# Kernel optimization log

Hardware: AMD Instinct MI355X
Metric: run time of the kernel (lower is better)

## Reference

```python
import jax, jax.numpy as jnp
import numpy as np

ORDER = 8
POOL = 8
N_SIDE = 1 << ORDER          # 256
N_PIX = N_SIDE * N_SIDE      # 65536
PSQ = POOL * POOL            # 64
CHANNEL = 2 * PSQ            # 128
PATH_NUM = N_PIX // PSQ      # 1024


def hilbert_indices(order):
    """hil[d] = row-major pixel index of the d-th point on the Hilbert curve;
    rehil = inverse permutation (rehil[hil[d]] = d)."""
    n = 1 << order
    d = np.arange(n * n, dtype=np.int64)
    x = np.zeros_like(d)
    y = np.zeros_like(d)
    t = d.copy()
    s = 1
    while s < n:
        rx = 1 & (t // 2)
        ry = 1 & (t ^ rx)
        swap = ry == 0
        flip = swap & (rx == 1)
        x = np.where(flip, s - 1 - x, x)
        y = np.where(flip, s - 1 - y, y)
        x, y = np.where(swap, y, x), np.where(swap, x, y)
        x = x + s * rx
        y = y + s * ry
        t = t // 4
        s *= 2
    hil = (y * n + x).astype(np.int32)
    rehil = np.argsort(hil).astype(np.int32)
    return hil, rehil


def setup_inputs() -> dict:
    key = jax.random.key(0)
    ks = jax.random.split(key, 10)
    b, c = 8, 128
    scale = 1.0 / np.sqrt(CHANNEL)
    hil, rehil = hilbert_indices(ORDER)
    return {
        "x": jax.random.normal(ks[0], (b, c, N_SIDE, N_SIDE), jnp.float32),
        "Wq": jax.random.normal(ks[1], (CHANNEL, CHANNEL), jnp.float32) * scale,
        "bq": jax.random.normal(ks[2], (CHANNEL,), jnp.float32) * 0.01,
        "Wk": jax.random.normal(ks[3], (CHANNEL, CHANNEL), jnp.float32) * scale,
        "bk": jax.random.normal(ks[4], (CHANNEL,), jnp.float32) * 0.01,
        "Wv": jax.random.normal(ks[5], (CHANNEL, CHANNEL), jnp.float32) * scale,
        "bv": jax.random.normal(ks[6], (CHANNEL,), jnp.float32) * 0.01,
        "Wpre": jax.random.normal(ks[7], (1, 2), jnp.float32) * 0.5,
        "bpre": jax.random.normal(ks[8], (1,), jnp.float32) * 0.01,
        "hil": jnp.asarray(hil),
        "rehil": jnp.asarray(rehil),
    }


def reference(x, Wq, bq, Wk, bk, Wv, bv, Wpre, bpre, hil, rehil):
    b, c, h, w = x.shape
    n_pix = h * w
    psq = Wq.shape[0] // 2
    path_num = n_pix // psq

    # channel-pooled descriptor: (b, 2, h*w)
    mean = jnp.mean(x, axis=1)
    mx = jnp.max(x, axis=1)
    x1 = jnp.stack([mean, mx], axis=1).reshape(b, 2, n_pix)

    # Hilbert-curve gather reorder of pixels
    xh = x1[:, :, hil]                                            # (b, 2, n_pix)

    # group psq consecutive curve points into one token of dim 2*psq
    feat = xh.reshape(b, 2, path_num, psq)
    feat = feat.transpose(0, 1, 3, 2).reshape(b, 2 * psq, path_num)  # (b, C, P)

    # 1x1-conv QKV projections
    Q = jnp.einsum('oc,bcp->bop', Wq, feat) + bq[None, :, None]
    K = jnp.einsum('oc,bcp->bop', Wk, feat) + bk[None, :, None]
    V = jnp.einsum('oc,bcp->bop', Wv, feat) + bv[None, :, None]

    # scores[b,p,q] = sum_c Q[b,c,p] * K[b,c,q]; softmax over dim 1 (as nn.Softmax(1))
    scores = jnp.einsum('bcp,bcq->bpq', Q, K)
    a = jax.nn.softmax(scores, axis=1)

    # x3c[b,c,p] = sum_q a[b,p,q] * V[b,c,q]
    x3c = jnp.einsum('bpq,bcq->bcp', a, V)                        # (b, C, P)

    # ungroup tokens back to curve order, then inverse-Hilbert scatter
    back = x3c.reshape(b, 2, psq, path_num).transpose(0, 1, 3, 2).reshape(b, 2, n_pix)
    restored = back[:, :, rehil].reshape(b, 2, h, w)

    # 1x1 conv 2 -> 1, sigmoid gate
    att = jnp.einsum('oc,bchw->bohw', Wpre, restored) + bpre[None, :, None, None]
    return jax.nn.sigmoid(att) * x
```

## Files before the change

### kernel.cpp

```cpp
#include <hip/hip_runtime.h>

#define BATCH 8
#define CH 128
#define NPIX 65536
#define PN 1024

__global__ __launch_bounds__(256) void k0_precompute(
    const float* __restrict__ Wq, const float* __restrict__ bq,
    const float* __restrict__ Wk, const float* __restrict__ bk,
    float* __restrict__ M, float* __restrict__ wqbk,
    float* __restrict__ wkbq, float* __restrict__ c0) {
  int t = blockIdx.x * 256 + threadIdx.x;
  if (t < 16384) {
    int c = t >> 7, c2 = t & 127;
    float s = 0.f;
    for (int o = 0; o < 128; ++o) s += Wq[o * 128 + c] * Wk[o * 128 + c2];
    M[t] = s;
  } else if (t < 16512) {
    int c = t - 16384;
    float s = 0.f;
    for (int o = 0; o < 128; ++o) s += Wq[o * 128 + c] * bk[o];
    wqbk[c] = s;
  } else if (t < 16640) {
    int c = t - 16512;
    float s = 0.f;
    for (int o = 0; o < 128; ++o) s += bq[o] * Wk[o * 128 + c];
    wkbq[c] = s;
  } else if (t == 16640) {
    float s = 0.f;
    for (int o = 0; o < 128; ++o) s += bq[o] * bk[o];
    c0[0] = s;
  }
}

__global__ __launch_bounds__(256) void k1_reduce_permute(
    const float* __restrict__ x, const int* __restrict__ rehil,
    float* __restrict__ F) {
  const int b = blockIdx.y;
  const int t = blockIdx.x * 256 + threadIdx.x;
  const int i0 = t * 4;
  const float* xb = x + (size_t)b * CH * NPIX + i0;
  float4 s = make_float4(0.f, 0.f, 0.f, 0.f);
  float4 m = make_float4(-1e30f, -1e30f, -1e30f, -1e30f);
  for (int c = 0; c < CH; ++c) {
    const float4 v = *(const float4*)(xb + (size_t)c * NPIX);
    s.x += v.x; s.y += v.y; s.z += v.z; s.w += v.w;
    m.x = fmaxf(m.x, v.x); m.y = fmaxf(m.y, v.y);
    m.z = fmaxf(m.z, v.z); m.w = fmaxf(m.w, v.w);
  }
  const float inv = 1.f / (float)CH;
  float mean[4] = {s.x * inv, s.y * inv, s.z * inv, s.w * inv};
  float mx[4] = {m.x, m.y, m.z, m.w};
  const int4 d4 = *(const int4*)(rehil + i0);
  int ds[4] = {d4.x, d4.y, d4.z, d4.w};
  float* Fb = F + (size_t)b * CH * PN;
#pragma unroll
  for (int e = 0; e < 4; ++e) {
    int d = ds[e];
    int p = d >> 6, j = d & 63;
    Fb[j * PN + p] = mean[e];
    Fb[(64 + j) * PN + p] = mx[e];
  }
}

__global__ __launch_bounds__(256) void ku_uv(
    const float* __restrict__ F, const float* __restrict__ wqbk,
    const float* __restrict__ wkbq, float* __restrict__ u, float* __restrict__ v) {
  const int b = blockIdx.y;
  const int p = blockIdx.x * 256 + threadIdx.x;
  const float* Fb = F + (size_t)b * CH * PN;
  float su = 0.f, sv = 0.f;
  for (int c = 0; c < CH; ++c) {
    float f = Fb[c * PN + p];
    su = fmaf(f, wqbk[c], su);
    sv = fmaf(f, wkbq[c], sv);
  }
  u[b * PN + p] = su;
  v[b * PN + p] = sv;
}

__global__ __launch_bounds__(256) void k2_gv(
    const float* __restrict__ M, const float* __restrict__ Wv,
    const float* __restrict__ bv, const float* __restrict__ F,
    float* __restrict__ G, float* __restrict__ Vt) {
  __shared__ float As[16][64];
  __shared__ float Bs[16][64];
  const int b = blockIdx.z;
  const int r0 = blockIdx.y * 64;
  const int q0 = blockIdx.x * 64;
  const float* Fb = F + (size_t)b * CH * PN;
  const int t = threadIdx.x;
  const int tx = t & 15, ty = t >> 4;
  const int arow = t & 63, ak4 = (t >> 6) * 4;
  float acc[4][4] = {};
  for (int k0 = 0; k0 < 128; k0 += 16) {
    const int r = r0 + arow;
    const float* Arow = (r < 128) ? (M + r * 128) : (Wv + (r - 128) * 128);
    float4 a = *(const float4*)(Arow + k0 + ak4);
    As[ak4 + 0][arow] = a.x;
    As[ak4 + 1][arow] = a.y;
    As[ak4 + 2][arow] = a.z;
    As[ak4 + 3][arow] = a.w;
    *(float4*)&Bs[ty][tx * 4] =
        *(const float4*)(Fb + (size_t)(k0 + ty) * PN + q0 + tx * 4);
    __syncthreads();
#pragma unroll
    for (int kk = 0; kk < 16; ++kk) {
      float4 a4 = *(const float4*)&As[kk][ty * 4];
      float4 b4 = *(const float4*)&Bs[kk][tx * 4];
      float av[4] = {a4.x, a4.y, a4.z, a4.w};
      float bw[4] = {b4.x, b4.y, b4.z, b4.w};
#pragma unroll
      for (int i = 0; i < 4; ++i)
#pragma unroll
        for (int j = 0; j < 4; ++j) acc[i][j] = fmaf(av[i], bw[j], acc[i][j]);
    }
    __syncthreads();
  }
  float* Gb = G + (size_t)b * CH * PN;
  float* Vtb = Vt + (size_t)b * PN * CH;
#pragma unroll
  for (int i = 0; i < 4; ++i) {
    const int r = r0 + ty * 4 + i;
#pragma unroll
    for (int j = 0; j < 4; ++j) {
      const int q = q0 + tx * 4 + j;
      if (r < 128) Gb[r * PN + q] = acc[i][j];
      else Vtb[(size_t)q * CH + (r - 128)] = acc[i][j] + bv[r - 128];
    }
  }
}

__global__ __launch_bounds__(256) void k3_scores(
    const float* __restrict__ G, const float* __restrict__ F,
    const float* __restrict__ u, const float* __restrict__ v,
    const float* __restrict__ c0, float* __restrict__ St) {
  __shared__ float As[16][64];
  __shared__ float Bs[16][64];
  const int b = blockIdx.z;
  const int q0 = blockIdx.y * 64;
  const int p0 = blockIdx.x * 64;
  const float* Gb = G + (size_t)b * CH * PN;
  const float* Fb = F + (size_t)b * CH * PN;
  const int t = threadIdx.x;
  const int tx = t & 15, ty = t >> 4;
  float acc[4][4] = {};
  for (int k0 = 0; k0 < 128; k0 += 16) {
    *(float4*)&As[ty][tx * 4] =
        *(const float4*)(Gb + (size_t)(k0 + ty) * PN + q0 + tx * 4);
    *(float4*)&Bs[ty][tx * 4] =
        *(const float4*)(Fb + (size_t)(k0 + ty) * PN + p0 + tx * 4);
    __syncthreads();
#pragma unroll
    for (int kk = 0; kk < 16; ++kk) {
      float4 a4 = *(const float4*)&As[kk][ty * 4];
      float4 b4 = *(const float4*)&Bs[kk][tx * 4];
      float av[4] = {a4.x, a4.y, a4.z, a4.w};
      float bw[4] = {b4.x, b4.y, b4.z, b4.w};
#pragma unroll
      for (int i = 0; i < 4; ++i)
#pragma unroll
        for (int j = 0; j < 4; ++j) acc[i][j] = fmaf(av[i], bw[j], acc[i][j]);
    }
    __syncthreads();
  }
  const float cc = c0[0];
  float* Sb = St + (size_t)b * PN * PN;
#pragma unroll
  for (int i = 0; i < 4; ++i) {
    const int q = q0 + ty * 4 + i;
    const float vq = v[b * PN + q] + cc;
#pragma unroll
    for (int j = 0; j < 4; ++j) {
      const int p = p0 + tx * 4 + j;
      Sb[(size_t)q * PN + p] = acc[i][j] + u[b * PN + p] + vq;
    }
  }
}

__global__ __launch_bounds__(256) void k4_softmax_stats(
    const float* __restrict__ St, float* __restrict__ mOut,
    float* __restrict__ izOut) {
  const int wid = threadIdx.x >> 6;
  const int lane = threadIdx.x & 63;
  const int row = blockIdx.x * 4 + wid;
  const float* Sr = St + (size_t)row * PN;
  float4 r[4];
  float m = -1e30f;
#pragma unroll
  for (int ch = 0; ch < 4; ++ch) {
    r[ch] = *(const float4*)(Sr + ch * 256 + lane * 4);
    m = fmaxf(m, fmaxf(fmaxf(r[ch].x, r[ch].y), fmaxf(r[ch].z, r[ch].w)));
  }
#pragma unroll
  for (int off = 32; off >= 1; off >>= 1) m = fmaxf(m, __shfl_xor(m, off));
  float z = 0.f;
#pragma unroll
  for (int ch = 0; ch < 4; ++ch) {
    z += __expf(r[ch].x - m) + __expf(r[ch].y - m) +
         __expf(r[ch].z - m) + __expf(r[ch].w - m);
  }
#pragma unroll
  for (int off = 32; off >= 1; off >>= 1) z += __shfl_xor(z, off);
  if (lane == 0) {
    mOut[row] = m;
    izOut[row] = 1.f / z;
  }
}

__global__ __launch_bounds__(256) void k5_av(
    const float* __restrict__ Vt, const float* __restrict__ St,
    const float* __restrict__ mIn, const float* __restrict__ izIn,
    float* __restrict__ X3) {
  __shared__ float As[16][64];
  __shared__ float Bs[16][64];
  const int b = blockIdx.z;
  const int c0 = blockIdx.y * 64;
  const int p0 = blockIdx.x * 64;
  const float* Vtb = Vt + (size_t)b * PN * CH;
  const float* Sb = St + (size_t)b * PN * PN;
  const int t = threadIdx.x;
  const int tx = t & 15, ty = t >> 4;
  float acc[4][4] = {};
  for (int k0 = 0; k0 < PN; k0 += 16) {
    const int q = k0 + ty;
    *(float4*)&As[ty][tx * 4] =
        *(const float4*)(Vtb + (size_t)q * CH + c0 + tx * 4);
    const float mq = mIn[b * PN + q];
    const float iz = izIn[b * PN + q];
    const float4 sv = *(const float4*)(Sb + (size_t)q * PN + p0 + tx * 4);
    float4 ev;
    ev.x = __expf(sv.x - mq) * iz;
    ev.y = __expf(sv.y - mq) * iz;
    ev.z = __expf(sv.z - mq) * iz;
    ev.w = __expf(sv.w - mq) * iz;
    *(float4*)&Bs[ty][tx * 4] = ev;
    __syncthreads();
#pragma unroll
    for (int kk = 0; kk < 16; ++kk) {
      float4 a4 = *(const float4*)&As[kk][ty * 4];
      float4 b4 = *(const float4*)&Bs[kk][tx * 4];
      float av[4] = {a4.x, a4.y, a4.z, a4.w};
      float bw[4] = {b4.x, b4.y, b4.z, b4.w};
#pragma unroll
      for (int i = 0; i < 4; ++i)
#pragma unroll
        for (int j = 0; j < 4; ++j) acc[i][j] = fmaf(av[i], bw[j], acc[i][j]);
    }
    __syncthreads();
  }
  float* X3b = X3 + (size_t)b * CH * PN;
#pragma unroll
  for (int i = 0; i < 4; ++i)
#pragma unroll
    for (int j = 0; j < 4; ++j)
      X3b[(size_t)(c0 + ty * 4 + i) * PN + p0 + tx * 4 + j] = acc[i][j];
}

__global__ __launch_bounds__(256) void k7_out(
    const float* __restrict__ x, const int* __restrict__ rehil,
    const float* __restrict__ X3, const float* __restrict__ Wpre,
    const float* __restrict__ bpre, float* __restrict__ out) {
  const int b = blockIdx.y;
  const int t = blockIdx.x * 256 + threadIdx.x;
  const int i0 = t * 4;
  const float w0 = Wpre[0], w1 = Wpre[1], b0 = bpre[0];
  const int4 d4 = *(const int4*)(rehil + i0);
  const float* X3b = X3 + (size_t)b * CH * PN;
  int ds[4] = {d4.x, d4.y, d4.z, d4.w};
  float g[4];
#pragma unroll
  for (int e = 0; e < 4; ++e) {
    const int d = ds[e];
    const int p = d >> 6, j = d & 63;
    const float r0v = X3b[j * PN + p];
    const float r1v = X3b[(64 + j) * PN + p];
    const float logit = fmaf(w0, r0v, fmaf(w1, r1v, b0));
    g[e] = 1.f / (1.f + __expf(-logit));
  }
  const size_t base = (size_t)b * CH * NPIX + i0;
#pragma unroll 4
  for (int c = 0; c < CH; ++c) {
    const float4 v = *(const float4*)(x + base + (size_t)c * NPIX);
    float4 o;
    o.x = v.x * g[0];
    o.y = v.y * g[1];
    o.z = v.z * g[2];
    o.w = v.w * g[3];
    *(float4*)(out + base + (size_t)c * NPIX) = o;
  }
}

extern "C" void kernel_launch(void* const* d_in, const int* in_sizes, int n_in,
                              void* d_out, int out_size, void* d_ws,
                              size_t ws_size, hipStream_t stream) {
  const float* x = (const float*)d_in[0];
  const float* Wq = (const float*)d_in[1];
  const float* bq = (const float*)d_in[2];
  const float* Wk = (const float*)d_in[3];
  const float* bk = (const float*)d_in[4];
  const float* Wv = (const float*)d_in[5];
  const float* bv = (const float*)d_in[6];
  const float* Wpre = (const float*)d_in[7];
  const float* bpre = (const float*)d_in[8];
  const int* rehil = (const int*)d_in[10];
  float* out = (float*)d_out;
  float* ws = (float*)d_ws;

  const size_t SZ_FEAT = (size_t)BATCH * CH * PN;
  float* F = ws;
  float* G = F + SZ_FEAT;
  float* Vt = G + SZ_FEAT;
  float* X3 = Vt + SZ_FEAT;
  float* Mw = X3 + SZ_FEAT;
  float* wqbk = Mw + 16384;
  float* wkbq = wqbk + 128;
  float* c0w = wkbq + 128;
  float* uw = c0w + 64;
  float* vw = uw + 8192;
  float* mw = vw + 8192;
  float* izw = mw + 8192;
  float* Stw = izw + 8192;
  const size_t need = (size_t)(Stw - ws) + (size_t)BATCH * PN * PN;
  float* St = Stw;
  if (ws_size < need * sizeof(float)) {
    St = out;
  }

  k0_precompute<<<66, 256, 0, stream>>>(Wq, bq, Wk, bk, Mw, wqbk, wkbq, c0w);
  k1_reduce_permute<<<dim3(64, BATCH), 256, 0, stream>>>(x, rehil, F);
  ku_uv<<<dim3(4, BATCH), 256, 0, stream>>>(F, wqbk, wkbq, uw, vw);
  k2_gv<<<dim3(16, 4, BATCH), 256, 0, stream>>>(Mw, Wv, bv, F, G, Vt);
  k3_scores<<<dim3(16, 16, BATCH), 256, 0, stream>>>(G, F, uw, vw, c0w, St);
  k4_softmax_stats<<<2048, 256, 0, stream>>>(St, mw, izw);
  k5_av<<<dim3(16, 2, BATCH), 256, 0, stream>>>(Vt, St, mw, izw, X3);
  k7_out<<<dim3(64, BATCH), 256, 0, stream>>>(x, rehil, X3, Wpre, bpre, out);
}
```

Measured before the change: 685.9 us.

## Use 128x128 register tiles and split-K attention-value matmul with separate reduction

```diff
diff --git a/kernel.cpp b/kernel.cpp
--- a/kernel.cpp
+++ b/kernel.cpp
@@ -131,49 +131,64 @@
   }
 }
 
-__global__ __launch_bounds__(256) void k3_scores(
+__global__ __launch_bounds__(256) void k3_scores128(
     const float* __restrict__ G, const float* __restrict__ F,
     const float* __restrict__ u, const float* __restrict__ v,
     const float* __restrict__ c0, float* __restrict__ St) {
-  __shared__ float As[16][64];
-  __shared__ float Bs[16][64];
+  __shared__ float As[16][128];
+  __shared__ float Bs[16][128];
   const int b = blockIdx.z;
-  const int q0 = blockIdx.y * 64;
-  const int p0 = blockIdx.x * 64;
+  const int q0 = blockIdx.y * 128;
+  const int p0 = blockIdx.x * 128;
   const float* Gb = G + (size_t)b * CH * PN;
   const float* Fb = F + (size_t)b * CH * PN;
   const int t = threadIdx.x;
   const int tx = t & 15, ty = t >> 4;
-  float acc[4][4] = {};
+  const int sr = t >> 4;
+  const int sc = (t & 15) * 8;
+  float acc[8][8] = {};
   for (int k0 = 0; k0 < 128; k0 += 16) {
-    *(float4*)&As[ty][tx * 4] =
-        *(const float4*)(Gb + (size_t)(k0 + ty) * PN + q0 + tx * 4);
-    *(float4*)&Bs[ty][tx * 4] =
-        *(const float4*)(Fb + (size_t)(k0 + ty) * PN + p0 + tx * 4);
+    const float* gsrc = Gb + (size_t)(k0 + sr) * PN + q0 + sc;
+    const float* fsrc = Fb + (size_t)(k0 + sr) * PN + p0 + sc;
+    *(float4*)&As[sr][sc] = *(const float4*)gsrc;
+    *(float4*)&As[sr][sc + 4] = *(const float4*)(gsrc + 4);
+    *(float4*)&Bs[sr][sc] = *(const float4*)fsrc;
+    *(float4*)&Bs[sr][sc + 4] = *(const float4*)(fsrc + 4);
     __syncthreads();
 #pragma unroll
     for (int kk = 0; kk < 16; ++kk) {
-      float4 a4 = *(const float4*)&As[kk][ty * 4];
-      float4 b4 = *(const float4*)&Bs[kk][tx * 4];
-      float av[4] = {a4.x, a4.y, a4.z, a4.w};
-      float bw[4] = {b4.x, b4.y, b4.z, b4.w};
-#pragma unroll
-      for (int i = 0; i < 4; ++i)
-#pragma unroll
-        for (int j = 0; j < 4; ++j) acc[i][j] = fmaf(av[i], bw[j], acc[i][j]);
+      float a0[8], b0[8];
+      *(float4*)&a0[0] = *(const float4*)&As[kk][ty * 4];
+      *(float4*)&a0[4] = *(const float4*)&As[kk][64 + ty * 4];
+      *(float4*)&b0[0] = *(const float4*)&Bs[kk][tx * 4];
+      *(float4*)&b0[4] = *(const float4*)&Bs[kk][64 + tx * 4];
+#pragma unroll
+      for (int i = 0; i < 8; ++i)
+#pragma unroll
+        for (int j = 0; j < 8; ++j) acc[i][j] = fmaf(a0[i], b0[j], acc[i][j]);
     }
     __syncthreads();
   }
   const float cc = c0[0];
   float* Sb = St + (size_t)b * PN * PN;
-#pragma unroll
-  for (int i = 0; i < 4; ++i) {
-    const int q = q0 + ty * 4 + i;
-    const float vq = v[b * PN + q] + cc;
-#pragma unroll
-    for (int j = 0; j < 4; ++j) {
-      const int p = p0 + tx * 4 + j;
-      Sb[(size_t)q * PN + p] = acc[i][j] + u[b * PN + p] + vq;
+  const float* ub = u + b * PN;
+  const float* vb = v + b * PN;
+  float4 u0 = *(const float4*)(ub + p0 + tx * 4);
+  float4 u1 = *(const float4*)(ub + p0 + 64 + tx * 4);
+  float ua[8] = {u0.x, u0.y, u0.z, u0.w, u1.x, u1.y, u1.z, u1.w};
+#pragma unroll
+  for (int i = 0; i < 8; ++i) {
+    const int q = q0 + ((i < 4) ? (ty * 4 + i) : (64 + ty * 4 + i - 4));
+    const float vq = vb[q] + cc;
+    float* row = Sb + (size_t)q * PN;
+#pragma unroll
+    for (int jh = 0; jh < 2; ++jh) {
+      float4 o;
+      o.x = acc[i][jh * 4 + 0] + ua[jh * 4 + 0] + vq;
+      o.y = acc[i][jh * 4 + 1] + ua[jh * 4 + 1] + vq;
+      o.z = acc[i][jh * 4 + 2] + ua[jh * 4 + 2] + vq;
+      o.w = acc[i][jh * 4 + 3] + ua[jh * 4 + 3] + vq;
+      *(float4*)(row + p0 + jh * 64 + tx * 4) = o;
     }
   }
 }
@@ -208,59 +223,92 @@
   }
 }
 
-__global__ __launch_bounds__(256) void k5_av(
+__global__ __launch_bounds__(256) void k5_av128(
     const float* __restrict__ Vt, const float* __restrict__ St,
     const float* __restrict__ mIn, const float* __restrict__ izIn,
-    float* __restrict__ X3) {
-  __shared__ float As[16][64];
-  __shared__ float Bs[16][64];
+    float* __restrict__ P) {
+  __shared__ float As[16][128];
+  __shared__ float Bs[16][128];
   const int b = blockIdx.z;
-  const int c0 = blockIdx.y * 64;
-  const int p0 = blockIdx.x * 64;
+  const int part = blockIdx.y;
+  const int p0 = blockIdx.x * 128;
   const float* Vtb = Vt + (size_t)b * PN * CH;
   const float* Sb = St + (size_t)b * PN * PN;
+  const float* mb = mIn + b * PN;
+  const float* izb = izIn + b * PN;
   const int t = threadIdx.x;
   const int tx = t & 15, ty = t >> 4;
-  float acc[4][4] = {};
-  for (int k0 = 0; k0 < PN; k0 += 16) {
-    const int q = k0 + ty;
-    *(float4*)&As[ty][tx * 4] =
-        *(const float4*)(Vtb + (size_t)q * CH + c0 + tx * 4);
-    const float mq = mIn[b * PN + q];
-    const float iz = izIn[b * PN + q];
-    const float4 sv = *(const float4*)(Sb + (size_t)q * PN + p0 + tx * 4);
-    float4 ev;
-    ev.x = __expf(sv.x - mq) * iz;
-    ev.y = __expf(sv.y - mq) * iz;
-    ev.z = __expf(sv.z - mq) * iz;
-    ev.w = __expf(sv.w - mq) * iz;
-    *(float4*)&Bs[ty][tx * 4] = ev;
+  const int sr = t >> 4;
+  const int sc = (t & 15) * 8;
+  float acc[8][8] = {};
+  const int qbase = part * 128;
+  for (int k0 = 0; k0 < 128; k0 += 16) {
+    const int q = qbase + k0 + sr;
+    const float* asrc = Vtb + (size_t)q * CH + sc;
+    *(float4*)&As[sr][sc] = *(const float4*)asrc;
+    *(float4*)&As[sr][sc + 4] = *(const float4*)(asrc + 4);
+    const float mq = mb[q];
+    const float iz = izb[q];
+    const float* ssrc = Sb + (size_t)q * PN + p0 + sc;
+    float4 s0 = *(const float4*)ssrc;
+    float4 s1 = *(const float4*)(ssrc + 4);
+    float4 e0, e1;
+    e0.x = __expf(s0.x - mq) * iz; e0.y = __expf(s0.y - mq) * iz;
+    e0.z = __expf(s0.z - mq) * iz; e0.w = __expf(s0.w - mq) * iz;
+    e1.x = __expf(s1.x - mq) * iz; e1.y = __expf(s1.y - mq) * iz;
+    e1.z = __expf(s1.z - mq) * iz; e1.w = __expf(s1.w - mq) * iz;
+    *(float4*)&Bs[sr][sc] = e0;
+    *(float4*)&Bs[sr][sc + 4] = e1;
     __syncthreads();
 #pragma unroll
     for (int kk = 0; kk < 16; ++kk) {
-      float4 a4 = *(const float4*)&As[kk][ty * 4];
-      float4 b4 = *(const float4*)&Bs[kk][tx * 4];
-      float av[4] = {a4.x, a4.y, a4.z, a4.w};
-      float bw[4] = {b4.x, b4.y, b4.z, b4.w};
-#pragma unroll
-      for (int i = 0; i < 4; ++i)
-#pragma unroll
-        for (int j = 0; j < 4; ++j) acc[i][j] = fmaf(av[i], bw[j], acc[i][j]);
-    }
-    __syncthreads();
-  }
-  float* X3b = X3 + (size_t)b * CH * PN;
-#pragma unroll
-  for (int i = 0; i < 4; ++i)
-#pragma unroll
-    for (int j = 0; j < 4; ++j)
-      X3b[(size_t)(c0 + ty * 4 + i) * PN + p0 + tx * 4 + j] = acc[i][j];
-}
-
-__global__ __launch_bounds__(256) void k7_out(
-    const float* __restrict__ x, const int* __restrict__ rehil,
-    const float* __restrict__ X3, const float* __restrict__ Wpre,
-    const float* __restrict__ bpre, float* __restrict__ out) {
+      float a0[8], b0[8];
+      *(float4*)&a0[0] = *(const float4*)&As[kk][ty * 4];
+      *(float4*)&a0[4] = *(const float4*)&As[kk][64 + ty * 4];
+      *(float4*)&b0[0] = *(const float4*)&Bs[kk][tx * 4];
+      *(float4*)&b0[4] = *(const float4*)&Bs[kk][64 + tx * 4];
+#pragma unroll
+      for (int i = 0; i < 8; ++i)
+#pragma unroll
+        for (int j = 0; j < 8; ++j) acc[i][j] = fmaf(a0[i], b0[j], acc[i][j]);
+    }
+    __syncthreads();
+  }
+  float* Pb = P + ((size_t)(part * BATCH + b) * CH) * PN;
+#pragma unroll
+  for (int i = 0; i < 8; ++i) {
+    const int c = (i < 4) ? (ty * 4 + i) : (64 + ty * 4 + i - 4);
+    float* row = Pb + (size_t)c * PN;
+#pragma unroll
+    for (int jh = 0; jh < 2; ++jh) {
+      float4 o;
+      o.x = acc[i][jh * 4 + 0];
+      o.y = acc[i][jh * 4 + 1];
+      o.z = acc[i][jh * 4 + 2];
+      o.w = acc[i][jh * 4 + 3];
+      *(float4*)(row + p0 + jh * 64 + tx * 4) = o;
+    }
+  }
+}
+
+__global__ __launch_bounds__(256) void k6_reduce(
+    const float* __restrict__ P, float* __restrict__ X3) {
+  const size_t t = (size_t)blockIdx.x * 256 + threadIdx.x;
+  const size_t idx = t * 4;
+  const size_t stride = (size_t)BATCH * CH * PN;
+  float4 s = *(const float4*)(P + idx);
+#pragma unroll
+  for (int part = 1; part < 8; ++part) {
+    const float4 v = *(const float4*)(P + part * stride + idx);
+    s.x += v.x; s.y += v.y; s.z += v.z; s.w += v.w;
+  }
+  *(float4*)(X3 + idx) = s;
+}
+
+__global__ __launch_bounds__(256) void k6g_gate(
+    const float* __restrict__ X3, const int* __restrict__ rehil,
+    const float* __restrict__ Wpre, const float* __restrict__ bpre,
+    float* __restrict__ gate) {
   const int b = blockIdx.y;
   const int t = blockIdx.x * 256 + threadIdx.x;
   const int i0 = t * 4;
@@ -268,7 +316,8 @@
   const int4 d4 = *(const int4*)(rehil + i0);
   const float* X3b = X3 + (size_t)b * CH * PN;
   int ds[4] = {d4.x, d4.y, d4.z, d4.w};
-  float g[4];
+  float4 g;
+  float* gp = &g.x;
 #pragma unroll
   for (int e = 0; e < 4; ++e) {
     const int d = ds[e];
@@ -276,17 +325,27 @@
     const float r0v = X3b[j * PN + p];
     const float r1v = X3b[(64 + j) * PN + p];
     const float logit = fmaf(w0, r0v, fmaf(w1, r1v, b0));
-    g[e] = 1.f / (1.f + __expf(-logit));
-  }
+    gp[e] = 1.f / (1.f + __expf(-logit));
+  }
+  *(float4*)(gate + (size_t)b * NPIX + i0) = g;
+}
+
+__global__ __launch_bounds__(256) void k7_out(
+    const float* __restrict__ x, const float* __restrict__ gate,
+    float* __restrict__ out) {
+  const int b = blockIdx.y;
+  const int t = blockIdx.x * 256 + threadIdx.x;
+  const int i0 = t * 4;
+  const float4 g = *(const float4*)(gate + (size_t)b * NPIX + i0);
   const size_t base = (size_t)b * CH * NPIX + i0;
 #pragma unroll 4
   for (int c = 0; c < CH; ++c) {
     const float4 v = *(const float4*)(x + base + (size_t)c * NPIX);
     float4 o;
-    o.x = v.x * g[0];
-    o.y = v.y * g[1];
-    o.z = v.z * g[2];
-    o.w = v.w * g[3];
+    o.x = v.x * g.x;
+    o.y = v.y * g.y;
+    o.z = v.z * g.z;
+    o.w = v.w * g.w;
     *(float4*)(out + base + (size_t)c * NPIX) = o;
   }
 }
@@ -320,7 +379,9 @@
   float* vw = uw + 8192;
   float* mw = vw + 8192;
   float* izw = mw + 8192;
-  float* Stw = izw + 8192;
+  float* gatew = izw + 8192;
+  float* Pw = gatew + 524288;
+  float* Stw = Pw + 8 * SZ_FEAT;
   const size_t need = (size_t)(Stw - ws) + (size_t)BATCH * PN * PN;
   float* St = Stw;
   if (ws_size < need * sizeof(float)) {
@@ -331,8 +392,10 @@
   k1_reduce_permute<<<dim3(64, BATCH), 256, 0, stream>>>(x, rehil, F);
   ku_uv<<<dim3(4, BATCH), 256, 0, stream>>>(F, wqbk, wkbq, uw, vw);
   k2_gv<<<dim3(16, 4, BATCH), 256, 0, stream>>>(Mw, Wv, bv, F, G, Vt);
-  k3_scores<<<dim3(16, 16, BATCH), 256, 0, stream>>>(G, F, uw, vw, c0w, St);
+  k3_scores128<<<dim3(8, 8, BATCH), 256, 0, stream>>>(G, F, uw, vw, c0w, St);
   k4_softmax_stats<<<2048, 256, 0, stream>>>(St, mw, izw);
-  k5_av<<<dim3(16, 2, BATCH), 256, 0, stream>>>(Vt, St, mw, izw, X3);
-  k7_out<<<dim3(64, BATCH), 256, 0, stream>>>(x, rehil, X3, Wpre, bpre, out);
-}
+  k5_av128<<<dim3(8, 8, BATCH), 256, 0, stream>>>(Vt, St, mw, izw, Pw);
+  k6_reduce<<<1024, 256, 0, stream>>>(Pw, X3);
+  k6g_gate<<<dim3(64, BATCH), 256, 0, stream>>>(X3, rehil, Wpre, bpre, gatew);
+  k7_out<<<dim3(64, BATCH), 256, 0, stream>>>(x, gatew, out);
+}
```

Measured after the change: 690.1 us. About the same (+0.6%).
